# Performance work log

Measured on AMD Instinct MI355X. Metric: run time of the kernel, lower is better.

## Reference

```python
import jax, jax.numpy as jnp
from jax import lax
import numpy as np

WIN = 9
PAD = WIN // 2
DN = ('NCDHW', 'OIDHW', 'NCDHW')


def box_sum(x):
    """9x9x9 all-ones box sum (same padding), computed separably per axis.
    Matches the original dense depthwise conv3d with a ones kernel exactly in math."""
    C = x.shape[1]
    for axis in range(3):  # spatial axes D, H, W
        kshape = [1, 1, 1]
        kshape[axis] = WIN
        kernel = jnp.ones((C, 1, *kshape), dtype=x.dtype)
        padding = [(PAD, PAD) if i == axis else (0, 0) for i in range(3)]
        x = lax.conv_general_dilated(
            x, kernel, window_strides=(1, 1, 1), padding=padding,
            dimension_numbers=DN, feature_group_count=C)
    return x


def setup_inputs() -> dict:
    key = jax.random.key(0)
    k1, k2 = jax.random.split(key)
    shape = (2, 1, 160, 192, 160)
    y_true = jax.random.uniform(k1, shape, dtype=jnp.float32)
    y_pred = jax.random.uniform(k2, shape, dtype=jnp.float32)
    return {"y_true": y_true, "y_pred": y_pred}


def reference(y_true, y_pred):
    Ii, Ji = y_true, y_pred
    win_size = jnp.asarray(WIN ** 3, dtype=Ii.dtype)

    I_sum = box_sum(Ii)
    J_sum = box_sum(Ji)
    I2_sum = box_sum(Ii * Ii)
    J2_sum = box_sum(Ji * Ji)
    IJ_sum = box_sum(Ii * Ji)

    u_I = I_sum / win_size
    u_J = J_sum / win_size

    cross = IJ_sum - u_I * J_sum
    I_var = jnp.maximum(I2_sum - u_I * I_sum, 1e-05)
    J_var = jnp.maximum(J2_sum - u_J * J_sum, 1e-05)

    cc = cross * cross / (I_var * J_var + 1e-05)
    return -jnp.sum(cc)
```

## Files before the change

kernel.cpp:

```cpp
#include <hip/hip_runtime.h>
#include <hip/hip_fp16.h>

#define ND 2
#define DD 160
#define HH 192
#define WW 160
#define HW (HH * WW)
#define DHW (DD * HH * WW)

constexpr int TW  = 32;
constexpr int TH  = 16;
constexpr int HLO = TH + 8;
constexpr int FCH = 40;
constexpr int NCH = DD / FCH;
constexpr int NSL = FCH + 8;
constexpr int NR  = NSL / 2;

struct alignas(8)  h4 { __half2 lo, hi; };
struct alignas(16) h8 { __half2 a, b, c, d; };

__device__ __forceinline__ void slide4(const float x[12], float S[4]) {
    float f = ((x[0] + x[1]) + (x[2] + x[3]))
            + ((x[4] + x[5]) + (x[6] + x[7])) + x[8];
    S[0] = f;
    f += x[9]  - x[0]; S[1] = f;
    f += x[10] - x[1]; S[2] = f;
    f += x[11] - x[2]; S[3] = f;
}

__global__ __launch_bounds__(512)
void ncc_fused4(const float* __restrict__ I, const float* __restrict__ J,
                float* __restrict__ outp)
{
    __shared__ h8     sws[2][HLO][TW + 1];
    __shared__ h4     ring4[9][512];
    __shared__ __half ring1[9][512];
    __shared__ float  wred[8];

    const int tid = threadIdx.x;
    const int w0  = blockIdx.x * TW;
    const int h0  = blockIdx.y * TH;
    const int z   = blockIdx.z;
    const int n   = z >> 2;
    const int d0  = (z & 3) * FCH;

    const bool ajob = (tid < 384);
    const int  sl   = tid / 192;
    const int  rj   = tid - sl * 192;
    const int  arow = rj >> 3;
    const int  awg  = rj & 7;
    const int  agh  = h0 + arow - 4;
    const bool ahok = (agh >= 0) && (agh < HH);
    const int  agws = w0 + awg * 4 - 4;

    const int oh = tid >> 5;
    const int ow = tid & 31;
    const int h  = h0 + oh, w = w0 + ow;
    const float cW  = (float)(min(w + 4, WW - 1) - max(w - 4, 0) + 1);
    const float cH  = (float)(min(h + 4, HH - 1) - max(h - 4, 0) + 1);
    const float cHW = cW * cH;

    {
        h4 zz; zz.lo = __floats2half2_rn(0.f, 0.f); zz.hi = zz.lo;
        const __half z1 = __float2half(0.f);
        #pragma unroll
        for (int q = 0; q < 9; ++q) { ring4[q][tid] = zz; ring1[q][tid] = z1; }
    }

    float run0 = 0.f, run1 = 0.f, run2 = 0.f, run3 = 0.f, run4 = 0.f;
    float acc = 0.f;
    const float inv = 1.0f / 729.0f;

    float pa[12], pb[12];
    auto load_ab = [&](int rrt) {
        const int dd  = d0 - 4 + 2 * rrt + sl;
        const bool dok = (dd >= 0) && (dd < DD);
        const int rbase = (n * DD + dd) * HW + agh * WW;
        #pragma unroll
        for (int c = 0; c < 3; ++c) {
            const int gw = agws + 4 * c;
            float4 va = make_float4(0.f, 0.f, 0.f, 0.f), vb = va;
            if (dok && ahok && gw >= 0 && gw < WW) {
                va = *(const float4*)(I + rbase + gw);
                vb = *(const float4*)(J + rbase + gw);
                va.x -= 0.5f; va.y -= 0.5f; va.z -= 0.5f; va.w -= 0.5f;
                vb.x -= 0.5f; vb.y -= 0.5f; vb.z -= 0.5f; vb.w -= 0.5f;
            }
            *(float4*)&pa[4 * c] = va;
            *(float4*)&pb[4 * c] = vb;
        }
    };
    if (ajob) load_ab(0);

    #pragma unroll 1
    for (int g = 0; g < 3; ++g) {
        #pragma unroll
        for (int r = 0; r < 9; ++r) {
            const int rr = g * 9 + r;
            if (rr < NR) {
                const int s0  = 2 * rr;
                const int dd0 = d0 - 4 + s0;
                if (ajob) {
                    const int dd = dd0 + sl;
                    if (dd >= 0 && dd < DD) {
                        float S0[4], S1[4], S2[4], S3[4], S4[4], f[12];
                        slide4(pa, S0);
                        slide4(pb, S1);
                        #pragma unroll
                        for (int i = 0; i < 12; ++i) f[i] = pa[i] * pa[i];
                        slide4(f, S2);
                        #pragma unroll
                        for (int i = 0; i < 12; ++i) f[i] = pb[i] * pb[i];
                        slide4(f, S3);
                        #pragma unroll
                        for (int i = 0; i < 12; ++i) f[i] = pa[i] * pb[i];
                        slide4(f, S4);
                        #pragma unroll
                        for (int t = 0; t < 4; ++t) {
                            h8 e;
                            e.a = __floats2half2_rn(S0[t], S1[t]);
                            e.b = __floats2half2_rn(S2[t], S3[t]);
                            e.c = __floats2half2_rn(S4[t], 0.f);
                            e.d = __floats2half2_rn(0.f, 0.f);
                            sws[sl][arow][awg * 4 + t] = e;
                        }
                    }
                    if (rr + 1 < NR) load_ab(rr + 1);
                }
                __syncthreads();
                #pragma unroll
                for (int half = 0; half < 2; ++half) {
                    const int s   = s0 + half;
                    const int ddx = dd0 + half;
                    __half2 a01 = __floats2half2_rn(0.f, 0.f);
                    __half2 a23 = a01, a4 = a01;
                    if (ddx >= 0 && ddx < DD) {
                        #pragma unroll
                        for (int q = 0; q < 9; ++q) {
                            const h8 v = sws[half][oh + q][ow];
                            a01 = __hadd2(a01, v.a);
                            a23 = __hadd2(a23, v.b);
                            a4  = __hadd2(a4,  v.c);
                        }
                    }
                    h4 nh; nh.lo = a01; nh.hi = a23;
                    const __half n4h = __low2half(a4);
                    const int jj = (2 * r + half) % 9;
                    const h4     po = ring4[jj][tid];
                    const __half p4 = ring1[jj][tid];
                    run0 += __low2float(nh.lo)  - __low2float(po.lo);
                    run1 += __high2float(nh.lo) - __high2float(po.lo);
                    run2 += __low2float(nh.hi)  - __low2float(po.hi);
                    run3 += __high2float(nh.hi) - __high2float(po.hi);
                    run4 += __half2float(n4h)   - __half2float(p4);
                    ring4[jj][tid] = nh;
                    ring1[jj][tid] = n4h;
                    if (s >= 8) {
                        const int d = d0 + s - 8;
                        const float cD  = (float)(min(d + 4, DD - 1) - max(d - 4, 0) + 1);
                        const float cnt = cHW * cD;
                        const float Is = run0 + 0.5f * cnt;
                        const float Js = run1 + 0.5f * cnt;
                        const float I2 = run2 + run0 + 0.25f * cnt;
                        const float J2 = run3 + run1 + 0.25f * cnt;
                        const float IJ = run4 + 0.5f * (run0 + run1) + 0.25f * cnt;
                        const float uI = Is * inv, uJ = Js * inv;
                        const float cross = IJ - uI * Js;
                        const float Iv = fmaxf(I2 - uI * Is, 1e-5f);
                        const float Jv = fmaxf(J2 - uJ * Js, 1e-5f);
                        acc += cross * cross / (Iv * Jv + 1e-5f);
                    }
                }
                __syncthreads();
            }
        }
    }

    #pragma unroll
    for (int off = 32; off > 0; off >>= 1)
        acc += __shfl_down(acc, off, 64);
    const int lane = tid & 63, wid = tid >> 6;
    if (lane == 0) wred[wid] = acc;
    __syncthreads();
    if (tid == 0) {
        float ssum = 0.f;
        #pragma unroll
        for (int i = 0; i < 8; ++i) ssum += wred[i];
        atomicAdd(outp, -ssum);
    }
}

extern "C" void kernel_launch(void* const* d_in, const int* in_sizes, int n_in,
                              void* d_out, int out_size, void* d_ws, size_t ws_size,
                              hipStream_t stream)
{
    const float* I = (const float*)d_in[0];
    const float* J = (const float*)d_in[1];
    float* out = (float*)d_out;

    hipMemsetAsync(out, 0, sizeof(float), stream);
    dim3 grid(WW / TW, HH / TH, ND * NCH);
    ncc_fused4<<<grid, 512, 0, stream>>>(I, J, out);
}
```

Before: 184.3 us.

## Process one depth slice per step with double-buffered fp32 W-sum staging

The kernel now processes one depth slice per iteration instead of two. A single group of 192 threads computes the W-direction sums and writes them as fp32 into a double-buffered shared array, for the next slice after the H-pass of the current one. This allows one barrier per slice, and the H-pass accumulates in fp32 instead of half2. The change removes fp16 accumulation error and overlaps production with consumption. In exchange it uses fewer producer threads, twice as many iterations and barriers, and more shared-memory traffic from the wider fp32 entries.

Result: slower. 193.3 us (+4.9%).

```diff
diff --git a/kernel.cpp b/kernel.cpp
--- a/kernel.cpp
+++ b/kernel.cpp
@@ -14,10 +14,8 @@
 constexpr int FCH = 40;
 constexpr int NCH = DD / FCH;
 constexpr int NSL = FCH + 8;
-constexpr int NR  = NSL / 2;
-
-struct alignas(8)  h4 { __half2 lo, hi; };
-struct alignas(16) h8 { __half2 a, b, c, d; };
+
+struct alignas(8) h4 { __half2 lo, hi; };
 
 __device__ __forceinline__ void slide4(const float x[12], float S[4]) {
     float f = ((x[0] + x[1]) + (x[2] + x[3]))
@@ -29,10 +27,11 @@
 }
 
 __global__ __launch_bounds__(512)
-void ncc_fused4(const float* __restrict__ I, const float* __restrict__ J,
+void ncc_fused5(const float* __restrict__ I, const float* __restrict__ J,
                 float* __restrict__ outp)
 {
-    __shared__ h8     sws[2][HLO][TW + 1];
+    __shared__ float4 sws[2][HLO][TW + 1];
+    __shared__ float  sw4[2][HLO][TW + 1];
     __shared__ h4     ring4[9][512];
     __shared__ __half ring1[9][512];
     __shared__ float  wred[8];
@@ -44,11 +43,9 @@
     const int n   = z >> 2;
     const int d0  = (z & 3) * FCH;
 
-    const bool ajob = (tid < 384);
-    const int  sl   = tid / 192;
-    const int  rj   = tid - sl * 192;
-    const int  arow = rj >> 3;
-    const int  awg  = rj & 7;
+    const bool ajob = (tid < 192);
+    const int  arow = tid >> 3;
+    const int  awg  = tid & 7;
     const int  agh  = h0 + arow - 4;
     const bool ahok = (agh >= 0) && (agh < HH);
     const int  agws = w0 + awg * 4 - 4;
@@ -72,8 +69,8 @@
     const float inv = 1.0f / 729.0f;
 
     float pa[12], pb[12];
-    auto load_ab = [&](int rrt) {
-        const int dd  = d0 - 4 + 2 * rrt + sl;
+    auto load_ab = [&](int ss) {
+        const int dd  = d0 - 4 + ss;
         const bool dok = (dd >= 0) && (dd < DD);
         const int rbase = (n * DD + dd) * HW + agh * WW;
         #pragma unroll
@@ -90,73 +87,69 @@
             *(float4*)&pb[4 * c] = vb;
         }
     };
-    if (ajob) load_ab(0);
+    auto consume_store = [&](int ss) {
+        const int dd = d0 - 4 + ss;
+        if (dd >= 0 && dd < DD) {
+            const int buf = ss & 1;
+            float S0[4], S1[4], S2[4], S3[4], S4[4], f[12];
+            slide4(pa, S0);
+            slide4(pb, S1);
+            #pragma unroll
+            for (int i = 0; i < 12; ++i) f[i] = pa[i] * pa[i];
+            slide4(f, S2);
+            #pragma unroll
+            for (int i = 0; i < 12; ++i) f[i] = pb[i] * pb[i];
+            slide4(f, S3);
+            #pragma unroll
+            for (int i = 0; i < 12; ++i) f[i] = pa[i] * pb[i];
+            slide4(f, S4);
+            #pragma unroll
+            for (int t = 0; t < 4; ++t) {
+                sws[buf][arow][awg * 4 + t] =
+                    make_float4(S0[t], S1[t], S2[t], S3[t]);
+                sw4[buf][arow][awg * 4 + t] = S4[t];
+            }
+        }
+    };
+
+    if (ajob) { load_ab(0); consume_store(0); }
+    __syncthreads();
 
     #pragma unroll 1
-    for (int g = 0; g < 3; ++g) {
+    for (int g = 0; g < 6; ++g) {
         #pragma unroll
         for (int r = 0; r < 9; ++r) {
             const int rr = g * 9 + r;
-            if (rr < NR) {
-                const int s0  = 2 * rr;
-                const int dd0 = d0 - 4 + s0;
-                if (ajob) {
-                    const int dd = dd0 + sl;
-                    if (dd >= 0 && dd < DD) {
-                        float S0[4], S1[4], S2[4], S3[4], S4[4], f[12];
-                        slide4(pa, S0);
-                        slide4(pb, S1);
-                        #pragma unroll
-                        for (int i = 0; i < 12; ++i) f[i] = pa[i] * pa[i];
-                        slide4(f, S2);
-                        #pragma unroll
-                        for (int i = 0; i < 12; ++i) f[i] = pb[i] * pb[i];
-                        slide4(f, S3);
-                        #pragma unroll
-                        for (int i = 0; i < 12; ++i) f[i] = pa[i] * pb[i];
-                        slide4(f, S4);
-                        #pragma unroll
-                        for (int t = 0; t < 4; ++t) {
-                            h8 e;
-                            e.a = __floats2half2_rn(S0[t], S1[t]);
-                            e.b = __floats2half2_rn(S2[t], S3[t]);
-                            e.c = __floats2half2_rn(S4[t], 0.f);
-                            e.d = __floats2half2_rn(0.f, 0.f);
-                            sws[sl][arow][awg * 4 + t] = e;
-                        }
-                    }
-                    if (rr + 1 < NR) load_ab(rr + 1);
-                }
-                __syncthreads();
-                #pragma unroll
-                for (int half = 0; half < 2; ++half) {
-                    const int s   = s0 + half;
-                    const int ddx = dd0 + half;
-                    __half2 a01 = __floats2half2_rn(0.f, 0.f);
-                    __half2 a23 = a01, a4 = a01;
+            if (rr < NSL) {
+                if (ajob && rr + 1 < NSL) load_ab(rr + 1);
+
+                {
+                    const int buf = rr & 1;
+                    const int ddx = d0 - 4 + rr;
+                    float t0 = 0.f, t1 = 0.f, t2 = 0.f, t3 = 0.f, t4 = 0.f;
                     if (ddx >= 0 && ddx < DD) {
                         #pragma unroll
                         for (int q = 0; q < 9; ++q) {
-                            const h8 v = sws[half][oh + q][ow];
-                            a01 = __hadd2(a01, v.a);
-                            a23 = __hadd2(a23, v.b);
-                            a4  = __hadd2(a4,  v.c);
+                            const float4 v = sws[buf][oh + q][ow];
+                            t0 += v.x; t1 += v.y; t2 += v.z; t3 += v.w;
+                            t4 += sw4[buf][oh + q][ow];
                         }
                     }
-                    h4 nh; nh.lo = a01; nh.hi = a23;
-                    const __half n4h = __low2half(a4);
-                    const int jj = (2 * r + half) % 9;
-                    const h4     po = ring4[jj][tid];
-                    const __half p4 = ring1[jj][tid];
+                    h4 nh;
+                    nh.lo = __floats2half2_rn(t0, t1);
+                    nh.hi = __floats2half2_rn(t2, t3);
+                    const __half n4h = __float2half(t4);
+                    const h4     po = ring4[r][tid];
+                    const __half p4 = ring1[r][tid];
                     run0 += __low2float(nh.lo)  - __low2float(po.lo);
                     run1 += __high2float(nh.lo) - __high2float(po.lo);
                     run2 += __low2float(nh.hi)  - __low2float(po.hi);
                     run3 += __high2float(nh.hi) - __high2float(po.hi);
                     run4 += __half2float(n4h)   - __half2float(p4);
-                    ring4[jj][tid] = nh;
-                    ring1[jj][tid] = n4h;
-                    if (s >= 8) {
-                        const int d = d0 + s - 8;
+                    ring4[r][tid] = nh;
+                    ring1[r][tid] = n4h;
+                    if (rr >= 8) {
+                        const int d = d0 + rr - 8;
                         const float cD  = (float)(min(d + 4, DD - 1) - max(d - 4, 0) + 1);
                         const float cnt = cHW * cD;
                         const float Is = run0 + 0.5f * cnt;
@@ -171,6 +164,9 @@
                         acc += cross * cross / (Iv * Jv + 1e-5f);
                     }
                 }
+
+                if (ajob && rr + 1 < NSL) consume_store(rr + 1);
+
                 __syncthreads();
             }
         }
@@ -200,5 +196,5 @@
 
     hipMemsetAsync(out, 0, sizeof(float), stream);
     dim3 grid(WW / TW, HH / TH, ND * NCH);
-    ncc_fused4<<<grid, 512, 0, stream>>>(I, J, out);
+    ncc_fused5<<<grid, 512, 0, stream>>>(I, J, out);
 }
```
